# Performance work log

Hardware: AMD Instinct MI355X
Metric: run time of the kernel (lower is better)

## Reference

```python
import jax, jax.numpy as jnp
import numpy as np

B, D, H, W, C = 2, 8, 64, 64, 128
NH = 8
WS = (2, 8, 8)
SS = (1, 4, 4)
HEAD_DIM = C // NH
SCALE = HEAD_DIM ** -0.5
MLP_HIDDEN = 4 * C


def _window_partition(x, ws):
    # x: (B, D, H, W, C) -> (B*nW, ws0*ws1*ws2, C)
    b, d, h, w, c = x.shape
    x = x.reshape(b, d // ws[0], ws[0], h // ws[1], ws[1], w // ws[2], ws[2], c)
    return x.transpose(0, 1, 3, 5, 2, 4, 6, 7).reshape(-1, ws[0] * ws[1] * ws[2], c)


def _window_reverse(win, ws, b, d, h, w):
    x = win.reshape(b, d // ws[0], h // ws[1], w // ws[2], ws[0], ws[1], ws[2], -1)
    return x.transpose(0, 1, 4, 2, 5, 3, 6, 7).reshape(b, d, h, w, -1)


def _rel_pos_index(ws):
    coords = np.stack(np.meshgrid(np.arange(ws[0]), np.arange(ws[1]), np.arange(ws[2]), indexing='ij'))
    cf = coords.reshape(3, -1)                       # (3, N)
    rel = (cf[:, :, None] - cf[:, None, :]).transpose(1, 2, 0)  # (N, N, 3)
    rel[:, :, 0] += ws[0] - 1
    rel[:, :, 1] += ws[1] - 1
    rel[:, :, 2] += ws[2] - 1
    rel[:, :, 0] *= (2 * ws[1] - 1) * (2 * ws[2] - 1)
    rel[:, :, 1] *= 2 * ws[2] - 1
    return rel.sum(-1)                               # (N, N)


def _attn_mask(d, h, w, ws, ss):
    img = np.zeros((1, d, h, w, 1), np.float32)
    cnt = 0
    for sd in (slice(-ws[0]), slice(-ws[0], -ss[0]), slice(-ss[0], None)):
        for sh in (slice(-ws[1]), slice(-ws[1], -ss[1]), slice(-ss[1], None)):
            for sw in (slice(-ws[2]), slice(-ws[2], -ss[2]), slice(-ss[2], None)):
                img[:, sd, sh, sw, :] = cnt
                cnt += 1
    mw = _window_partition(img, ws)[..., 0]          # (nW, N)
    am = mw[:, None, :] - mw[:, :, None]             # (nW, N, N)
    return np.where(am != 0, -100.0, 0.0).astype(np.float32)


def _ln(x, g, b):
    m = x.mean(-1, keepdims=True)
    v = ((x - m) ** 2).mean(-1, keepdims=True)
    return (x - m) / jnp.sqrt(v + 1e-5) * g + b


def setup_inputs() -> dict:
    key = jax.random.key(0)
    ks = jax.random.split(key, 8)
    n_bias = (2 * WS[0] - 1) * (2 * WS[1] - 1) * (2 * WS[2] - 1)
    return {
        'x': jax.random.normal(ks[0], (B, D, H, W, C), jnp.float32),
        'qkv_w': jax.random.normal(ks[1], (3 * C, C), jnp.float32) * 0.02,
        'qkv_b': jnp.zeros((3 * C,), jnp.float32),
        'proj_w': jax.random.normal(ks[2], (C, C), jnp.float32) * 0.02,
        'proj_b': jnp.zeros((C,), jnp.float32),
        'rpb': jax.random.normal(ks[3], (n_bias, NH), jnp.float32) * 0.02,
        'ln1_g': jnp.ones((C,), jnp.float32),
        'ln1_b': jnp.zeros((C,), jnp.float32),
        'ln2_g': jnp.ones((C,), jnp.float32),
        'ln2_b': jnp.zeros((C,), jnp.float32),
        'fc1_w': jax.random.normal(ks[4], (MLP_HIDDEN, C), jnp.float32) * 0.02,
        'fc1_b': jnp.zeros((MLP_HIDDEN,), jnp.float32),
        'fc2_w': jax.random.normal(ks[5], (C, MLP_HIDDEN), jnp.float32) * 0.02,
        'fc2_b': jnp.zeros((C,), jnp.float32),
    }


def reference(x, qkv_w, qkv_b, proj_w, proj_b, rpb, ln1_g, ln1_b, ln2_g, ln2_b, fc1_w, fc1_b, fc2_w, fc2_b):
    shortcut = x
    xn = _ln(x, ln1_g, ln1_b)
    # cyclic shift (SW-MSA)
    xs = jnp.roll(xn, (-SS[0], -SS[1], -SS[2]), axis=(1, 2, 3))
    win = _window_partition(xs, WS)                  # (Bw, N, C)
    Bw, N, _ = win.shape
    qkv = (win @ qkv_w.T + qkv_b).reshape(Bw, N, 3, NH, HEAD_DIM).transpose(2, 0, 3, 1, 4)
    q, k, v = qkv[0] * SCALE, qkv[1], qkv[2]         # (Bw, NH, N, d)
    attn = jnp.einsum('bhnd,bhmd->bhnm', q, k)       # (Bw, NH, N, N)
    rpi = _rel_pos_index(WS)
    bias = rpb[rpi.reshape(-1)].reshape(N, N, NH).transpose(2, 0, 1)  # (NH, N, N)
    attn = attn + bias[None]
    mask = jnp.asarray(_attn_mask(D, H, W, WS, SS))  # (nW, N, N)
    nW = mask.shape[0]
    attn = attn.reshape(B, nW, NH, N, N) + mask[None, :, None]
    attn = jax.nn.softmax(attn, axis=-1).reshape(Bw, NH, N, N)
    out = jnp.einsum('bhnm,bhmd->bhnd', attn, v).transpose(0, 2, 1, 3).reshape(Bw, N, C)
    out = out @ proj_w.T + proj_b
    xr = _window_reverse(out, WS, B, D, H, W)
    xr = jnp.roll(xr, SS, axis=(1, 2, 3))
    x1 = shortcut + xr
    # MLP block
    y = _ln(x1, ln2_g, ln2_b)
    y = jax.nn.gelu(y @ fc1_w.T + fc1_b, approximate=False)
    y = y @ fc2_w.T + fc2_b
    return x1 + y
```

## Files before the change

kernel.cpp:

```cpp
#include <hip/hip_runtime.h>
#include <math.h>

typedef short s16x8 __attribute__((ext_vector_type(8)));
typedef float f32x4 __attribute__((ext_vector_type(4)));

#define MFMA(a, b, c)   __builtin_amdgcn_mfma_f32_16x16x32_bf16(a, b, c, 0, 0, 0)

__device__ __forceinline__ float b2f(ushort u) {
    union { unsigned int i; float f; } v; v.i = ((unsigned int)u) << 16; return v.f;
}
__device__ __forceinline__ ushort f2b(float f) {
    union { float f; unsigned int i; } v; v.f = f;
    unsigned int r = v.i + 0x7fffu + ((v.i >> 16) & 1u);
    return (ushort)(r >> 16);
}

__global__ __launch_bounds__(256) void k0a_prep(
    const float* __restrict__ qkv_w, const float* __restrict__ proj_w,
    const float* __restrict__ rpb, ushort* __restrict__ T)
{
    int tid = threadIdx.x;
    if (blockIdx.x < 256) {
        int idx = blockIdx.x * 256 + tid;
        float v = (idx < 49152) ? qkv_w[idx] : proj_w[idx - 49152];
        T[idx] = f2b(v);
        return;
    }
    int bi = blockIdx.x - 256;
    int cls = bi >> 3, head = bi & 7;
    int ed = (cls >> 2) & 1, eh = (cls >> 1) & 1, ew = cls & 1;
    int j = tid & 127;
    int tdj = j >> 6, thj = (j >> 3) & 7, twj = j & 7;
    int regj = (ed ? (tdj + 1) : 0) * 9
             + (eh ? ((thj < 4) ? 1 : 2) : 0) * 3
             + (ew ? ((twj < 4) ? 1 : 2) : 0);
    ushort* bm = T + 65536 + (long)bi * 16384;
    for (int ii = 0; ii < 64; ++ii) {
        int i = (tid >> 7) * 64 + ii;
        int tdi = i >> 6, thi = (i >> 3) & 7, twi = i & 7;
        int regi = (ed ? (tdi + 1) : 0) * 9
                 + (eh ? ((thi < 4) ? 1 : 2) : 0) * 3
                 + (ew ? ((twi < 4) ? 1 : 2) : 0);
        int rpi = (tdi - tdj + 1) * 225 + (thi - thj + 7) * 15 + (twi - twj + 7);
        float v = rpb[rpi * 8 + head] + ((regi != regj) ? -100.f : 0.f);
        bm[i * 128 + j] = f2b(v);
    }
}

__global__ __launch_bounds__(256) void k0b_wconv(
    const float* __restrict__ fc1_w, const float* __restrict__ fc2_w,
    ushort* __restrict__ wf)
{
    int idx = blockIdx.x * 256 + threadIdx.x;
    float v = (idx < 65536) ? fc1_w[idx] : fc2_w[idx - 65536];
    wf[idx] = f2b(v);
}

__global__ __launch_bounds__(256) void k2_qkv(
    const float* __restrict__ x, const float* __restrict__ g,
    const float* __restrict__ be, const ushort* __restrict__ wq,
    const float* __restrict__ qkv_b, ushort* __restrict__ qkv)
{
    __shared__ __align__(16) ushort As[128][136];
    int tid = threadIdx.x;
    int m0 = blockIdx.x * 128;
    {
        int row = tid >> 1, half = tid & 1;
        int tk = m0 + row;
        int wi = tk >> 7, t = tk & 127;
        int b = wi >> 8, wd = (wi >> 6) & 3, wh = (wi >> 3) & 7, ww = wi & 7;
        int td = t >> 6, th = (t >> 3) & 7, tw = t & 7;
        int d = (wd * 2 + td + 1) & 7;
        int h = (wh * 8 + th + 4) & 63;
        int w = (ww * 8 + tw + 4) & 63;
        long src = (((long)((b * 8 + d) * 64 + h)) * 64 + w) * 128 + half * 64;
        float vals[64];
        float s = 0.f, q = 0.f;
        #pragma unroll
        for (int i = 0; i < 16; ++i) {
            float4 u = *(const float4*)&x[src + i * 4];
            vals[i * 4 + 0] = u.x; vals[i * 4 + 1] = u.y;
            vals[i * 4 + 2] = u.z; vals[i * 4 + 3] = u.w;
            s += u.x + u.y + u.z + u.w;
            q += u.x * u.x + u.y * u.y + u.z * u.z + u.w * u.w;
        }
        s += __shfl_xor(s, 1);
        q += __shfl_xor(q, 1);
        float mean = s * (1.f / 128.f);
        float rstd = rsqrtf(q * (1.f / 128.f) - mean * mean + 1e-5f);
        #pragma unroll
        for (int i = 0; i < 8; ++i) {
            ushort pk[8];
            #pragma unroll
            for (int jj = 0; jj < 8; ++jj) {
                int c = half * 64 + i * 8 + jj;
                pk[jj] = f2b((vals[i * 8 + jj] - mean) * rstd * g[c] + be[c]);
            }
            *(uint4*)&As[row][half * 64 + i * 8] = *(uint4*)pk;
        }
    }
    __syncthreads();
    int wv = tid >> 6, lane = tid & 63, li = lane & 15, quad = lane >> 4;
    int wm = wv >> 1, wn = wv & 1;
    for (int nb = 0; nb < 3; ++nb) {
        f32x4 acc[4][4] = {};
        for (int s = 0; s < 4; ++s) {
            s16x8 a[4], bw[4];
            #pragma unroll
            for (int mi = 0; mi < 4; ++mi)
                a[mi] = *(const s16x8*)&As[wm * 64 + mi * 16 + li][s * 32 + quad * 8];
            #pragma unroll
            for (int ni = 0; ni < 4; ++ni)
                bw[ni] = *(const s16x8*)&wq[(long)(nb * 128 + wn * 64 + ni * 16 + li) * 128
                                            + s * 32 + quad * 8];
            #pragma unroll
            for (int mi = 0; mi < 4; ++mi)
                #pragma unroll
                for (int ni = 0; ni < 4; ++ni)
                    acc[mi][ni] = MFMA(a[mi], bw[ni], acc[mi][ni]);
        }
        #pragma unroll
        for (int mi = 0; mi < 4; ++mi)
            #pragma unroll
            for (int ni = 0; ni < 4; ++ni) {
                int gcol = nb * 128 + wn * 64 + ni * 16 + li;
                int mat = gcol >> 7, hd = (gcol >> 4) & 7;
                float bias = qkv_b[gcol];
                float scale = (mat == 0) ? 0.25f : 1.f;
                #pragma unroll
                for (int r = 0; r < 4; ++r) {
                    int grow = m0 + wm * 64 + mi * 16 + quad * 4 + r;
                    qkv[((long)(mat * 8 + hd) * 65536 + grow) * 16 + li] =
                        f2b((acc[mi][ni][r] + bias) * scale);
                }
            }
    }
}

__global__ __launch_bounds__(256) void k3_attn(
    const ushort* __restrict__ qkv, const ushort* __restrict__ bm,
    ushort* __restrict__ ao)
{
    __shared__ __align__(16) ushort qs[128][40];
    __shared__ __align__(16) ushort ks[128][40];
    __shared__ __align__(16) ushort vt[16][136];
    __shared__ __align__(16) ushort ps[128][136];
    int bid = blockIdx.x;
    int wi = bid >> 3, head = bid & 7;
    int wd = (wi >> 6) & 3, wh = (wi >> 3) & 7, ww = wi & 7;
    int cls = ((wd == 3) << 2) | ((wh == 7) << 1) | (ww == 7);
    long bmbase = (long)(cls * 8 + head) * 16384;
    int tid = threadIdx.x;
    int wv = tid >> 6, lane = tid & 63, li = lane & 15, quad = lane >> 4;
    {
        int token = tid >> 1, dd0 = (tid & 1) * 8;
        long tb = (long)(wi * 128 + token) * 16 + dd0;
        uint4 qv = *(const uint4*)&qkv[(long)head * 1048576 + tb];
        uint4 kv = *(const uint4*)&qkv[(long)(8 + head) * 1048576 + tb];
        uint4 vv = *(const uint4*)&qkv[(long)(16 + head) * 1048576 + tb];
        uint4 z = {0, 0, 0, 0};
        *(uint4*)&qs[token][dd0] = qv;
        *(uint4*)&ks[token][dd0] = kv;
        *(uint4*)&qs[token][16 + dd0] = z;
        *(uint4*)&ks[token][16 + dd0] = z;
        const ushort* pv = (const ushort*)&vv;
        #pragma unroll
        for (int j = 0; j < 8; ++j) vt[dd0 + j][token] = pv[j];
    }
    __syncthreads();
    f32x4 sacc[2][8] = {};
    s16x8 a[2];
    #pragma unroll
    for (int mi = 0; mi < 2; ++mi)
        a[mi] = *(const s16x8*)&qs[wv * 32 + mi * 16 + li][quad * 8];
    #pragma unroll
    for (int ni = 0; ni < 8; ++ni) {
        s16x8 bf = *(const s16x8*)&ks[ni * 16 + li][quad * 8];
        #pragma unroll
        for (int mi = 0; mi < 2; ++mi) sacc[mi][ni] = MFMA(a[mi], bf, sacc[mi][ni]);
    }
    #pragma unroll
    for (int mi = 0; mi < 2; ++mi) {
        #pragma unroll
        for (int r = 0; r < 4; ++r) {
            int i = wv * 32 + mi * 16 + quad * 4 + r;
            float sv[8];
            float rowmax = -1e30f;
            #pragma unroll
            for (int ni = 0; ni < 8; ++ni) {
                float v = sacc[mi][ni][r] + b2f(bm[bmbase + i * 128 + ni * 16 + li]);
                sv[ni] = v;
                rowmax = fmaxf(rowmax, v);
            }
            #pragma unroll
            for (int m = 1; m < 16; m <<= 1) rowmax = fmaxf(rowmax, __shfl_xor(rowmax, m));
            float sum = 0.f;
            #pragma unroll
            for (int ni = 0; ni < 8; ++ni) { sv[ni] = __expf(sv[ni] - rowmax); sum += sv[ni]; }
            #pragma unroll
            for (int m = 1; m < 16; m <<= 1) sum += __shfl_xor(sum, m);
            float inv = 1.f / sum;
            #pragma unroll
            for (int ni = 0; ni < 8; ++ni) ps[i][ni * 16 + li] = f2b(sv[ni] * inv);
        }
    }
    __syncthreads();
    f32x4 pacc[2] = {};
    #pragma unroll
    for (int kk = 0; kk < 4; ++kk) {
        s16x8 bv = *(const s16x8*)&vt[li][kk * 32 + quad * 8];
        #pragma unroll
        for (int mi = 0; mi < 2; ++mi) {
            s16x8 ap = *(const s16x8*)&ps[wv * 32 + mi * 16 + li][kk * 32 + quad * 8];
            pacc[mi] = MFMA(ap, bv, pacc[mi]);
        }
    }
    #pragma unroll
    for (int mi = 0; mi < 2; ++mi)
        #pragma unroll
        for (int r = 0; r < 4; ++r) {
            int i = wv * 32 + mi * 16 + quad * 4 + r;
            ao[((long)(wi * 128 + i)) * 128 + head * 16 + li] = f2b(pacc[mi][r]);
        }
}

__global__ __launch_bounds__(256) void k4_proj(
    const ushort* __restrict__ ao, const ushort* __restrict__ wp,
    const float* __restrict__ proj_b, const float* __restrict__ x,
    ushort* __restrict__ x1)
{
    __shared__ __align__(16) ushort As[128][136];
    int tid = threadIdx.x;
    int m0 = blockIdx.x * 128;
    #pragma unroll
    for (int i = 0; i < 8; ++i) {
        int slot = tid + i * 256;
        int row = slot >> 4, col8 = (slot & 15) * 8;
        *(uint4*)&As[row][col8] = *(const uint4*)&ao[(long)(m0 + row) * 128 + col8];
    }
    __syncthreads();
    int wv = tid >> 6, lane = tid & 63, li = lane & 15, quad = lane >> 4;
    int wm = wv >> 1, wn = wv & 1;
    f32x4 acc[4][4] = {};
    for (int s = 0; s < 4; ++s) {
        s16x8 a[4], bw[4];
        #pragma unroll
        for (int mi = 0; mi < 4; ++mi)
            a[mi] = *(const s16x8*)&As[wm * 64 + mi * 16 + li][s * 32 + quad * 8];
        #pragma unroll
        for (int ni = 0; ni < 4; ++ni)
            bw[ni] = *(const s16x8*)&wp[(long)(wn * 64 + ni * 16 + li) * 128 + s * 32 + quad * 8];
        #pragma unroll
        for (int mi = 0; mi < 4; ++mi)
            #pragma unroll
            for (int ni = 0; ni < 4; ++ni)
                acc[mi][ni] = MFMA(a[mi], bw[ni], acc[mi][ni]);
    }
    #pragma unroll
    for (int mi = 0; mi < 4; ++mi) {
        #pragma unroll
        for (int r = 0; r < 4; ++r) {
            int grow = m0 + wm * 64 + mi * 16 + quad * 4 + r;
            int wi2 = grow >> 7, t = grow & 127;
            int b = wi2 >> 8, wd = (wi2 >> 6) & 3, wh = (wi2 >> 3) & 7, ww = wi2 & 7;
            int td = t >> 6, th = (t >> 3) & 7, tw = t & 7;
            int d = (wd * 2 + td + 1) & 7, h = (wh * 8 + th + 4) & 63, w = (ww * 8 + tw + 4) & 63;
            long di = (((long)((b * 8 + d) * 64 + h)) * 64 + w) * 128;
            #pragma unroll
            for (int ni = 0; ni < 4; ++ni) {
                int gcol = wn * 64 + ni * 16 + li;
                x1[di + gcol] = f2b(acc[mi][ni][r] + proj_b[gcol] + x[di + gcol]);
            }
        }
    }
}

__global__ __launch_bounds__(256) void k5_mlp(
    const ushort* __restrict__ x1, const float* __restrict__ g2,
    const float* __restrict__ be2, const ushort* __restrict__ wf1,
    const float* __restrict__ fc1_b, const ushort* __restrict__ wf2,
    const float* __restrict__ fc2_b, float* __restrict__ out)
{
    __shared__ __align__(16) ushort xs[64][136];
    __shared__ __align__(16) ushort hs[64][136];
    __shared__ float redS[4][64];
    __shared__ float redQ[4][64];
    int tid = threadIdx.x;
    int m0 = blockIdx.x * 64;
    int wv = tid >> 6, lane = tid & 63, li = lane & 15, quad = lane >> 4;
    int wm = wv >> 1, wn = wv & 1;
    {
        int token = tid & 63, part = tid >> 6;
        float vals[32];
        float s = 0.f, q = 0.f;
        #pragma unroll
        for (int i = 0; i < 4; ++i) {
            uint4 u = *(const uint4*)&x1[(long)(m0 + token) * 128 + part * 32 + i * 8];
            const ushort* p = (const ushort*)&u;
            #pragma unroll
            for (int j = 0; j < 8; ++j) { float f = b2f(p[j]); vals[i * 8 + j] = f; s += f; q += f * f; }
        }
        redS[part][token] = s; redQ[part][token] = q;
        __syncthreads();
        float st = 0.f, qt = 0.f;
        #pragma unroll
        for (int p2 = 0; p2 < 4; ++p2) { st += redS[p2][token]; qt += redQ[p2][token]; }
        float mean = st * (1.f / 128.f);
        float rstd = rsqrtf(qt * (1.f / 128.f) - mean * mean + 1e-5f);
        #pragma unroll
        for (int i = 0; i < 4; ++i) {
            ushort packed[8];
            #pragma unroll
            for (int j = 0; j < 8; ++j) {
                int c = part * 32 + i * 8 + j;
                packed[j] = f2b((vals[i * 8 + j] - mean) * rstd * g2[c] + be2[c]);
            }
            *(uint4*)&xs[token][part * 32 + i * 8] = *(uint4*)packed;
        }
    }
    __syncthreads();

    f32x4 yacc[2][4] = {};
    for (int hc = 0; hc < 4; ++hc) {
        f32x4 hacc[2][4] = {};
        #pragma unroll
        for (int kk = 0; kk < 4; ++kk) {
            s16x8 a[2], bw[4];
            #pragma unroll
            for (int mi = 0; mi < 2; ++mi)
                a[mi] = *(const s16x8*)&xs[wm * 32 + mi * 16 + li][kk * 32 + quad * 8];
            #pragma unroll
            for (int ni = 0; ni < 4; ++ni)
                bw[ni] = *(const s16x8*)&wf1[(long)(hc * 128 + wn * 64 + ni * 16 + li) * 128
                                             + kk * 32 + quad * 8];
            #pragma unroll
            for (int mi = 0; mi < 2; ++mi)
                #pragma unroll
                for (int ni = 0; ni < 4; ++ni)
                    hacc[mi][ni] = MFMA(a[mi], bw[ni], hacc[mi][ni]);
        }
        #pragma unroll
        for (int mi = 0; mi < 2; ++mi)
            #pragma unroll
            for (int ni = 0; ni < 4; ++ni) {
                int col = wn * 64 + ni * 16 + li;
                float bb = fc1_b[hc * 128 + col];
                #pragma unroll
                for (int r = 0; r < 4; ++r) {
                    int row = wm * 32 + mi * 16 + quad * 4 + r;
                    float v = hacc[mi][ni][r] + bb;
                    hs[row][col] = f2b(0.5f * v * (1.f + erff(v * 0.70710678118f)));
                }
            }
        __syncthreads();
        #pragma unroll
        for (int kk = 0; kk < 4; ++kk) {
            s16x8 a[2], bw[4];
            #pragma unroll
            for (int mi = 0; mi < 2; ++mi)
                a[mi] = *(const s16x8*)&hs[wm * 32 + mi * 16 + li][kk * 32 + quad * 8];
            #pragma unroll
            for (int ni = 0; ni < 4; ++ni)
                bw[ni] = *(const s16x8*)&wf2[(long)(wn * 64 + ni * 16 + li) * 512
                                             + hc * 128 + kk * 32 + quad * 8];
            #pragma unroll
            for (int mi = 0; mi < 2; ++mi)
                #pragma unroll
                for (int ni = 0; ni < 4; ++ni)
                    yacc[mi][ni] = MFMA(a[mi], bw[ni], yacc[mi][ni]);
        }
        __syncthreads();
    }
    #pragma unroll
    for (int mi = 0; mi < 2; ++mi)
        #pragma unroll
        for (int ni = 0; ni < 4; ++ni) {
            int col = wn * 64 + ni * 16 + li;
            float fb = fc2_b[col];
            #pragma unroll
            for (int r = 0; r < 4; ++r) {
                int row = wm * 32 + mi * 16 + quad * 4 + r;
                long idx = (long)(m0 + row) * 128 + col;
                out[idx] = b2f(x1[idx]) + yacc[mi][ni][r] + fb;
            }
        }
}

extern "C" void kernel_launch(void* const* d_in, const int* in_sizes, int n_in,
                              void* d_out, int out_size, void* d_ws, size_t ws_size,
                              hipStream_t stream)
{
    (void)in_sizes; (void)n_in; (void)out_size; (void)ws_size;
    const float* x      = (const float*)d_in[0];
    const float* qkv_w  = (const float*)d_in[1];
    const float* qkv_b  = (const float*)d_in[2];
    const float* proj_w = (const float*)d_in[3];
    const float* proj_b = (const float*)d_in[4];
    const float* rpb    = (const float*)d_in[5];
    const float* ln1_g  = (const float*)d_in[6];
    const float* ln1_b  = (const float*)d_in[7];
    const float* ln2_g  = (const float*)d_in[8];
    const float* ln2_b  = (const float*)d_in[9];
    const float* fc1_w  = (const float*)d_in[10];
    const float* fc1_b  = (const float*)d_in[11];
    const float* fc2_w  = (const float*)d_in[12];
    const float* fc2_b  = (const float*)d_in[13];
    float* out = (float*)d_out;

    ushort* qkvb = (ushort*)d_ws;
    ushort* x1b  = (ushort*)d_ws;
    ushort* wf   = (ushort*)((char*)d_ws + 33554432);
    ushort* aob  = (ushort*)d_out;
    ushort* T    = (ushort*)d_out + 8388608;
    ushort* wq   = T;
    ushort* wp   = T + 49152;
    ushort* bm   = T + 65536;

    hipLaunchKernelGGL(k0a_prep, dim3(320), dim3(256), 0, stream, qkv_w, proj_w, rpb, T);
    hipLaunchKernelGGL(k2_qkv,   dim3(512), dim3(256), 0, stream, x, ln1_g, ln1_b, wq, qkv_b, qkvb);
    hipLaunchKernelGGL(k3_attn,  dim3(4096), dim3(256), 0, stream, qkvb, bm, aob);
    hipLaunchKernelGGL(k0b_wconv, dim3(512), dim3(256), 0, stream, fc1_w, fc2_w, wf);
    hipLaunchKernelGGL(k4_proj,  dim3(512), dim3(256), 0, stream, aob, wp, proj_b, x, x1b);
    hipLaunchKernelGGL(k5_mlp,   dim3(1024), dim3(256), 0, stream,
                       x1b, ln2_g, ln2_b, wf, fc1_b, wf + 65536, fc2_b, out);
}
```

Baseline: 288.0 us.

## Fuse proj and MLP kernels, loop heads per window block, merge prep kernels

Merges the two weight-prep kernels into one launch and changes the qkv layout to per-window contiguous storage. The attention kernel now handles all 8 heads of a window in one block and writes its output in place over the qkv buffer. The projection and MLP kernels are fused so x1 stays in shared memory instead of round-tripping through global memory. GELU switches from erf to a tanh approximation, which saves work but departs from the reference's exact GELU and may change accuracy.

```diff
diff --git a/kernel.cpp b/kernel.cpp
--- a/kernel.cpp
+++ b/kernel.cpp
@@ -14,19 +14,29 @@
     unsigned int r = v.i + 0x7fffu + ((v.i >> 16) & 1u);
     return (ushort)(r >> 16);
 }
-
-__global__ __launch_bounds__(256) void k0a_prep(
+__device__ __forceinline__ float gelu_tanh(float v) {
+    float u = 0.7978845608f * (v + 0.044715f * v * v * v);
+    float e = __expf(-2.f * fabsf(u));
+    float t = (1.f - e) / (1.f + e);
+    t = (u < 0.f) ? -t : t;
+    return 0.5f * v * (1.f + t);
+}
+
+__global__ __launch_bounds__(256) void k0_prep(
     const float* __restrict__ qkv_w, const float* __restrict__ proj_w,
-    const float* __restrict__ rpb, ushort* __restrict__ T)
+    const float* __restrict__ fc1_w, const float* __restrict__ fc2_w,
+    const float* __restrict__ rpb, ushort* __restrict__ wq,
+    ushort* __restrict__ wp, ushort* __restrict__ wf, ushort* __restrict__ bm)
 {
-    int tid = threadIdx.x;
-    if (blockIdx.x < 256) {
-        int idx = blockIdx.x * 256 + tid;
-        float v = (idx < 49152) ? qkv_w[idx] : proj_w[idx - 49152];
-        T[idx] = f2b(v);
+    int bid = blockIdx.x, tid = threadIdx.x;
+    if (bid < 192) { int idx = bid * 256 + tid; wq[idx] = f2b(qkv_w[idx]); return; }
+    if (bid < 256) { int idx = (bid - 192) * 256 + tid; wp[idx] = f2b(proj_w[idx]); return; }
+    if (bid < 768) {
+        int idx = (bid - 256) * 256 + tid;
+        wf[idx] = f2b(idx < 65536 ? fc1_w[idx] : fc2_w[idx - 65536]);
         return;
     }
-    int bi = blockIdx.x - 256;
+    int bi = bid - 768;
     int cls = bi >> 3, head = bi & 7;
     int ed = (cls >> 2) & 1, eh = (cls >> 1) & 1, ew = cls & 1;
     int j = tid & 127;
@@ -34,7 +44,7 @@
     int regj = (ed ? (tdj + 1) : 0) * 9
              + (eh ? ((thj < 4) ? 1 : 2) : 0) * 3
              + (ew ? ((twj < 4) ? 1 : 2) : 0);
-    ushort* bm = T + 65536 + (long)bi * 16384;
+    ushort* bmp = bm + (long)bi * 16384;
     for (int ii = 0; ii < 64; ++ii) {
         int i = (tid >> 7) * 64 + ii;
         int tdi = i >> 6, thi = (i >> 3) & 7, twi = i & 7;
@@ -43,17 +53,8 @@
                  + (ew ? ((twi < 4) ? 1 : 2) : 0);
         int rpi = (tdi - tdj + 1) * 225 + (thi - thj + 7) * 15 + (twi - twj + 7);
         float v = rpb[rpi * 8 + head] + ((regi != regj) ? -100.f : 0.f);
-        bm[i * 128 + j] = f2b(v);
-    }
-}
-
-__global__ __launch_bounds__(256) void k0b_wconv(
-    const float* __restrict__ fc1_w, const float* __restrict__ fc2_w,
-    ushort* __restrict__ wf)
-{
-    int idx = blockIdx.x * 256 + threadIdx.x;
-    float v = (idx < 65536) ? fc1_w[idx] : fc2_w[idx - 65536];
-    wf[idx] = f2b(v);
+        bmp[i * 128 + j] = f2b(v);
+    }
 }
 
 __global__ __launch_bounds__(256) void k2_qkv(
@@ -102,6 +103,7 @@
     __syncthreads();
     int wv = tid >> 6, lane = tid & 63, li = lane & 15, quad = lane >> 4;
     int wm = wv >> 1, wn = wv & 1;
+    long wibase = (long)(m0 >> 7) * 49152;
     for (int nb = 0; nb < 3; ++nb) {
         f32x4 acc[4][4] = {};
         for (int s = 0; s < 4; ++s) {
@@ -127,175 +129,183 @@
                 int mat = gcol >> 7, hd = (gcol >> 4) & 7;
                 float bias = qkv_b[gcol];
                 float scale = (mat == 0) ? 0.25f : 1.f;
+                long base2 = wibase + mat * 16384 + hd * 2048 + li;
                 #pragma unroll
                 for (int r = 0; r < 4; ++r) {
-                    int grow = m0 + wm * 64 + mi * 16 + quad * 4 + r;
-                    qkv[((long)(mat * 8 + hd) * 65536 + grow) * 16 + li] =
-                        f2b((acc[mi][ni][r] + bias) * scale);
+                    int trow = wm * 64 + mi * 16 + quad * 4 + r;
+                    qkv[base2 + trow * 16] = f2b((acc[mi][ni][r] + bias) * scale);
                 }
             }
     }
 }
 
 __global__ __launch_bounds__(256) void k3_attn(
-    const ushort* __restrict__ qkv, const ushort* __restrict__ bm,
-    ushort* __restrict__ ao)
+    ushort* __restrict__ qkv, const ushort* __restrict__ bm)
 {
     __shared__ __align__(16) ushort qs[128][40];
     __shared__ __align__(16) ushort ks[128][40];
     __shared__ __align__(16) ushort vt[16][136];
     __shared__ __align__(16) ushort ps[128][136];
-    int bid = blockIdx.x;
-    int wi = bid >> 3, head = bid & 7;
+    int wi = blockIdx.x;
     int wd = (wi >> 6) & 3, wh = (wi >> 3) & 7, ww = wi & 7;
     int cls = ((wd == 3) << 2) | ((wh == 7) << 1) | (ww == 7);
-    long bmbase = (long)(cls * 8 + head) * 16384;
     int tid = threadIdx.x;
     int wv = tid >> 6, lane = tid & 63, li = lane & 15, quad = lane >> 4;
-    {
-        int token = tid >> 1, dd0 = (tid & 1) * 8;
-        long tb = (long)(wi * 128 + token) * 16 + dd0;
-        uint4 qv = *(const uint4*)&qkv[(long)head * 1048576 + tb];
-        uint4 kv = *(const uint4*)&qkv[(long)(8 + head) * 1048576 + tb];
-        uint4 vv = *(const uint4*)&qkv[(long)(16 + head) * 1048576 + tb];
-        uint4 z = {0, 0, 0, 0};
-        *(uint4*)&qs[token][dd0] = qv;
-        *(uint4*)&ks[token][dd0] = kv;
-        *(uint4*)&qs[token][16 + dd0] = z;
-        *(uint4*)&ks[token][16 + dd0] = z;
-        const ushort* pv = (const ushort*)&vv;
-        #pragma unroll
-        for (int j = 0; j < 8; ++j) vt[dd0 + j][token] = pv[j];
-    }
-    __syncthreads();
-    f32x4 sacc[2][8] = {};
-    s16x8 a[2];
+    long wbase = (long)wi * 49152;
+    uint2 opk[8][2];
+    for (int h = 0; h < 8; ++h) {
+        __syncthreads();
+        {   int token = tid >> 1, dd0 = (tid & 1) * 8;
+            long tb = wbase + h * 2048 + token * 16 + dd0;
+            uint4 qv = *(const uint4*)&qkv[tb];
+            uint4 kv = *(const uint4*)&qkv[tb + 16384];
+            uint4 vv = *(const uint4*)&qkv[tb + 32768];
+            uint4 z = {0, 0, 0, 0};
+            *(uint4*)&qs[token][dd0] = qv;
+            *(uint4*)&ks[token][dd0] = kv;
+            *(uint4*)&qs[token][16 + dd0] = z;
+            *(uint4*)&ks[token][16 + dd0] = z;
+            const ushort* pv = (const ushort*)&vv;
+            #pragma unroll
+            for (int j = 0; j < 8; ++j) vt[dd0 + j][token] = pv[j];
+        }
+        __syncthreads();
+        f32x4 sacc[2][8] = {};
+        s16x8 a[2];
+        #pragma unroll
+        for (int mi = 0; mi < 2; ++mi)
+            a[mi] = *(const s16x8*)&qs[wv * 32 + mi * 16 + li][quad * 8];
+        #pragma unroll
+        for (int ni = 0; ni < 8; ++ni) {
+            s16x8 bf = *(const s16x8*)&ks[ni * 16 + li][quad * 8];
+            #pragma unroll
+            for (int mi = 0; mi < 2; ++mi) sacc[mi][ni] = MFMA(a[mi], bf, sacc[mi][ni]);
+        }
+        long bmbase = (long)(cls * 8 + h) * 16384;
+        #pragma unroll
+        for (int mi = 0; mi < 2; ++mi) {
+            #pragma unroll
+            for (int r = 0; r < 4; ++r) {
+                int i = wv * 32 + mi * 16 + quad * 4 + r;
+                float sv[8];
+                float rowmax = -1e30f;
+                #pragma unroll
+                for (int ni = 0; ni < 8; ++ni) {
+                    float v = sacc[mi][ni][r] + b2f(bm[bmbase + i * 128 + ni * 16 + li]);
+                    sv[ni] = v;
+                    rowmax = fmaxf(rowmax, v);
+                }
+                #pragma unroll
+                for (int m = 1; m < 16; m <<= 1) rowmax = fmaxf(rowmax, __shfl_xor(rowmax, m));
+                float sum = 0.f;
+                #pragma unroll
+                for (int ni = 0; ni < 8; ++ni) { sv[ni] = __expf(sv[ni] - rowmax); sum += sv[ni]; }
+                #pragma unroll
+                for (int m = 1; m < 16; m <<= 1) sum += __shfl_xor(sum, m);
+                float inv = 1.f / sum;
+                #pragma unroll
+                for (int ni = 0; ni < 8; ++ni) ps[i][ni * 16 + li] = f2b(sv[ni] * inv);
+            }
+        }
+        __syncthreads();
+        f32x4 pacc[2] = {};
+        #pragma unroll
+        for (int kk = 0; kk < 4; ++kk) {
+            s16x8 bv = *(const s16x8*)&vt[li][kk * 32 + quad * 8];
+            #pragma unroll
+            for (int mi = 0; mi < 2; ++mi) {
+                s16x8 ap = *(const s16x8*)&ps[wv * 32 + mi * 16 + li][kk * 32 + quad * 8];
+                pacc[mi] = MFMA(ap, bv, pacc[mi]);
+            }
+        }
+        #pragma unroll
+        for (int mi = 0; mi < 2; ++mi) {
+            opk[h][mi].x = (unsigned int)f2b(pacc[mi][0]) | ((unsigned int)f2b(pacc[mi][1]) << 16);
+            opk[h][mi].y = (unsigned int)f2b(pacc[mi][2]) | ((unsigned int)f2b(pacc[mi][3]) << 16);
+        }
+    }
     #pragma unroll
-    for (int mi = 0; mi < 2; ++mi)
-        a[mi] = *(const s16x8*)&qs[wv * 32 + mi * 16 + li][quad * 8];
-    #pragma unroll
-    for (int ni = 0; ni < 8; ++ni) {
-        s16x8 bf = *(const s16x8*)&ks[ni * 16 + li][quad * 8];
-        #pragma unroll
-        for (int mi = 0; mi < 2; ++mi) sacc[mi][ni] = MFMA(a[mi], bf, sacc[mi][ni]);
-    }
-    #pragma unroll
-    for (int mi = 0; mi < 2; ++mi) {
-        #pragma unroll
-        for (int r = 0; r < 4; ++r) {
-            int i = wv * 32 + mi * 16 + quad * 4 + r;
-            float sv[8];
-            float rowmax = -1e30f;
-            #pragma unroll
-            for (int ni = 0; ni < 8; ++ni) {
-                float v = sacc[mi][ni][r] + b2f(bm[bmbase + i * 128 + ni * 16 + li]);
-                sv[ni] = v;
-                rowmax = fmaxf(rowmax, v);
-            }
-            #pragma unroll
-            for (int m = 1; m < 16; m <<= 1) rowmax = fmaxf(rowmax, __shfl_xor(rowmax, m));
-            float sum = 0.f;
-            #pragma unroll
-            for (int ni = 0; ni < 8; ++ni) { sv[ni] = __expf(sv[ni] - rowmax); sum += sv[ni]; }
-            #pragma unroll
-            for (int m = 1; m < 16; m <<= 1) sum += __shfl_xor(sum, m);
-            float inv = 1.f / sum;
-            #pragma unroll
-            for (int ni = 0; ni < 8; ++ni) ps[i][ni * 16 + li] = f2b(sv[ni] * inv);
-        }
-    }
-    __syncthreads();
-    f32x4 pacc[2] = {};
-    #pragma unroll
-    for (int kk = 0; kk < 4; ++kk) {
-        s16x8 bv = *(const s16x8*)&vt[li][kk * 32 + quad * 8];
+    for (int h = 0; h < 8; ++h)
         #pragma unroll
         for (int mi = 0; mi < 2; ++mi) {
-            s16x8 ap = *(const s16x8*)&ps[wv * 32 + mi * 16 + li][kk * 32 + quad * 8];
-            pacc[mi] = MFMA(ap, bv, pacc[mi]);
-        }
-    }
-    #pragma unroll
-    for (int mi = 0; mi < 2; ++mi)
-        #pragma unroll
-        for (int r = 0; r < 4; ++r) {
-            int i = wv * 32 + mi * 16 + quad * 4 + r;
-            ao[((long)(wi * 128 + i)) * 128 + head * 16 + li] = f2b(pacc[mi][r]);
-        }
-}
-
-__global__ __launch_bounds__(256) void k4_proj(
+            unsigned int w0 = opk[h][mi].x, w1 = opk[h][mi].y;
+            #pragma unroll
+            for (int r = 0; r < 4; ++r) {
+                unsigned int word = (r < 2) ? w0 : w1;
+                ushort v = (ushort)((word >> ((r & 1) * 16)) & 0xffff);
+                int i = wv * 32 + mi * 16 + quad * 4 + r;
+                qkv[wbase + (long)i * 128 + h * 16 + li] = v;
+            }
+        }
+}
+
+__global__ __launch_bounds__(256) void k45(
     const ushort* __restrict__ ao, const ushort* __restrict__ wp,
     const float* __restrict__ proj_b, const float* __restrict__ x,
-    ushort* __restrict__ x1)
+    const float* __restrict__ g2, const float* __restrict__ be2,
+    const ushort* __restrict__ wf1, const float* __restrict__ fc1_b,
+    const ushort* __restrict__ wf2, const float* __restrict__ fc2_b,
+    float* __restrict__ out)
 {
-    __shared__ __align__(16) ushort As[128][136];
+    __shared__ __align__(16) ushort As[64][132];
+    __shared__ __align__(16) ushort x1t[64][132];
+    __shared__ __align__(16) ushort hs[64][132];
+    __shared__ float redS[4][64];
+    __shared__ float redQ[4][64];
     int tid = threadIdx.x;
-    int m0 = blockIdx.x * 128;
+    int b = blockIdx.x;
+    int wi = b >> 1, half64 = b & 1;
+    int wd = (wi >> 6) & 3, wh = (wi >> 3) & 7, ww = wi & 7;
+    int bb = wi >> 8;
+    long aobase = (long)wi * 49152 + half64 * 8192;
     #pragma unroll
-    for (int i = 0; i < 8; ++i) {
+    for (int i = 0; i < 4; ++i) {
         int slot = tid + i * 256;
-        int row = slot >> 4, col8 = (slot & 15) * 8;
-        *(uint4*)&As[row][col8] = *(const uint4*)&ao[(long)(m0 + row) * 128 + col8];
+        int row = slot >> 4, c8 = (slot & 15) * 8;
+        *(uint4*)&As[row][c8] = *(const uint4*)&ao[aobase + row * 128 + c8];
     }
     __syncthreads();
     int wv = tid >> 6, lane = tid & 63, li = lane & 15, quad = lane >> 4;
     int wm = wv >> 1, wn = wv & 1;
-    f32x4 acc[4][4] = {};
+    f32x4 acc[2][4] = {};
     for (int s = 0; s < 4; ++s) {
-        s16x8 a[4], bw[4];
-        #pragma unroll
-        for (int mi = 0; mi < 4; ++mi)
-            a[mi] = *(const s16x8*)&As[wm * 64 + mi * 16 + li][s * 32 + quad * 8];
+        s16x8 a[2], bw[4];
+        #pragma unroll
+        for (int mi = 0; mi < 2; ++mi)
+            a[mi] = *(const s16x8*)&As[wm * 32 + mi * 16 + li][s * 32 + quad * 8];
         #pragma unroll
         for (int ni = 0; ni < 4; ++ni)
             bw[ni] = *(const s16x8*)&wp[(long)(wn * 64 + ni * 16 + li) * 128 + s * 32 + quad * 8];
         #pragma unroll
-        for (int mi = 0; mi < 4; ++mi)
+        for (int mi = 0; mi < 2; ++mi)
             #pragma unroll
             for (int ni = 0; ni < 4; ++ni)
                 acc[mi][ni] = MFMA(a[mi], bw[ni], acc[mi][ni]);
     }
     #pragma unroll
-    for (int mi = 0; mi < 4; ++mi) {
+    for (int mi = 0; mi < 2; ++mi) {
         #pragma unroll
         for (int r = 0; r < 4; ++r) {
-            int grow = m0 + wm * 64 + mi * 16 + quad * 4 + r;
-            int wi2 = grow >> 7, t = grow & 127;
-            int b = wi2 >> 8, wd = (wi2 >> 6) & 3, wh = (wi2 >> 3) & 7, ww = wi2 & 7;
+            int lrow = wm * 32 + mi * 16 + quad * 4 + r;
+            int t = half64 * 64 + lrow;
             int td = t >> 6, th = (t >> 3) & 7, tw = t & 7;
             int d = (wd * 2 + td + 1) & 7, h = (wh * 8 + th + 4) & 63, w = (ww * 8 + tw + 4) & 63;
-            long di = (((long)((b * 8 + d) * 64 + h)) * 64 + w) * 128;
+            long di = (((long)((bb * 8 + d) * 64 + h)) * 64 + w) * 128;
             #pragma unroll
             for (int ni = 0; ni < 4; ++ni) {
-                int gcol = wn * 64 + ni * 16 + li;
-                x1[di + gcol] = f2b(acc[mi][ni][r] + proj_b[gcol] + x[di + gcol]);
-            }
-        }
-    }
-}
-
-__global__ __launch_bounds__(256) void k5_mlp(
-    const ushort* __restrict__ x1, const float* __restrict__ g2,
-    const float* __restrict__ be2, const ushort* __restrict__ wf1,
-    const float* __restrict__ fc1_b, const ushort* __restrict__ wf2,
-    const float* __restrict__ fc2_b, float* __restrict__ out)
-{
-    __shared__ __align__(16) ushort xs[64][136];
-    __shared__ __align__(16) ushort hs[64][136];
-    __shared__ float redS[4][64];
-    __shared__ float redQ[4][64];
-    int tid = threadIdx.x;
-    int m0 = blockIdx.x * 64;
-    int wv = tid >> 6, lane = tid & 63, li = lane & 15, quad = lane >> 4;
-    int wm = wv >> 1, wn = wv & 1;
+                int col = wn * 64 + ni * 16 + li;
+                x1t[lrow][col] = f2b(acc[mi][ni][r] + proj_b[col] + x[di + col]);
+            }
+        }
+    }
+    __syncthreads();
     {
         int token = tid & 63, part = tid >> 6;
         float vals[32];
         float s = 0.f, q = 0.f;
         #pragma unroll
         for (int i = 0; i < 4; ++i) {
-            uint4 u = *(const uint4*)&x1[(long)(m0 + token) * 128 + part * 32 + i * 8];
+            uint4 u = *(const uint4*)&x1t[token][part * 32 + i * 8];
             const ushort* p = (const ushort*)&u;
             #pragma unroll
             for (int j = 0; j < 8; ++j) { float f = b2f(p[j]); vals[i * 8 + j] = f; s += f; q += f * f; }
@@ -315,11 +325,10 @@
                 int c = part * 32 + i * 8 + j;
                 packed[j] = f2b((vals[i * 8 + j] - mean) * rstd * g2[c] + be2[c]);
             }
-            *(uint4*)&xs[token][part * 32 + i * 8] = *(uint4*)packed;
+            *(uint4*)&As[token][part * 32 + i * 8] = *(uint4*)packed;
         }
     }
     __syncthreads();
-
     f32x4 yacc[2][4] = {};
     for (int hc = 0; hc < 4; ++hc) {
         f32x4 hacc[2][4] = {};
@@ -328,7 +337,7 @@
             s16x8 a[2], bw[4];
             #pragma unroll
             for (int mi = 0; mi < 2; ++mi)
-                a[mi] = *(const s16x8*)&xs[wm * 32 + mi * 16 + li][kk * 32 + quad * 8];
+                a[mi] = *(const s16x8*)&As[wm * 32 + mi * 16 + li][kk * 32 + quad * 8];
             #pragma unroll
             for (int ni = 0; ni < 4; ++ni)
                 bw[ni] = *(const s16x8*)&wf1[(long)(hc * 128 + wn * 64 + ni * 16 + li) * 128
@@ -344,12 +353,11 @@
             #pragma unroll
             for (int ni = 0; ni < 4; ++ni) {
                 int col = wn * 64 + ni * 16 + li;
-                float bb = fc1_b[hc * 128 + col];
+                float bbv = fc1_b[hc * 128 + col];
                 #pragma unroll
                 for (int r = 0; r < 4; ++r) {
                     int row = wm * 32 + mi * 16 + quad * 4 + r;
-                    float v = hacc[mi][ni][r] + bb;
-                    hs[row][col] = f2b(0.5f * v * (1.f + erff(v * 0.70710678118f)));
+                    hs[row][col] = f2b(gelu_tanh(hacc[mi][ni][r] + bbv));
                 }
             }
         __syncthreads();
@@ -372,18 +380,21 @@
         __syncthreads();
     }
     #pragma unroll
-    for (int mi = 0; mi < 2; ++mi)
-        #pragma unroll
-        for (int ni = 0; ni < 4; ++ni) {
-            int col = wn * 64 + ni * 16 + li;
-            float fb = fc2_b[col];
-            #pragma unroll
-            for (int r = 0; r < 4; ++r) {
-                int row = wm * 32 + mi * 16 + quad * 4 + r;
-                long idx = (long)(m0 + row) * 128 + col;
-                out[idx] = b2f(x1[idx]) + yacc[mi][ni][r] + fb;
-            }
-        }
+    for (int mi = 0; mi < 2; ++mi) {
+        #pragma unroll
+        for (int r = 0; r < 4; ++r) {
+            int lrow = wm * 32 + mi * 16 + quad * 4 + r;
+            int t = half64 * 64 + lrow;
+            int td = t >> 6, th = (t >> 3) & 7, tw = t & 7;
+            int d = (wd * 2 + td + 1) & 7, h = (wh * 8 + th + 4) & 63, w = (ww * 8 + tw + 4) & 63;
+            long di = (((long)((bb * 8 + d) * 64 + h)) * 64 + w) * 128;
+            #pragma unroll
+            for (int ni = 0; ni < 4; ++ni) {
+                int col = wn * 64 + ni * 16 + li;
+                out[di + col] = b2f(x1t[lrow][col]) + yacc[mi][ni][r] + fc2_b[col];
+            }
+        }
+    }
 }
 
 extern "C" void kernel_launch(void* const* d_in, const int* in_sizes, int n_in,
@@ -408,19 +419,17 @@
     float* out = (float*)d_out;
 
     ushort* qkvb = (ushort*)d_ws;
-    ushort* x1b  = (ushort*)d_ws;
-    ushort* wf   = (ushort*)((char*)d_ws + 33554432);
-    ushort* aob  = (ushort*)d_out;
-    ushort* T    = (ushort*)d_out + 8388608;
-    ushort* wq   = T;
-    ushort* wp   = T + 49152;
-    ushort* bm   = T + 65536;
-
-    hipLaunchKernelGGL(k0a_prep, dim3(320), dim3(256), 0, stream, qkv_w, proj_w, rpb, T);
-    hipLaunchKernelGGL(k2_qkv,   dim3(512), dim3(256), 0, stream, x, ln1_g, ln1_b, wq, qkv_b, qkvb);
-    hipLaunchKernelGGL(k3_attn,  dim3(4096), dim3(256), 0, stream, qkvb, bm, aob);
-    hipLaunchKernelGGL(k0b_wconv, dim3(512), dim3(256), 0, stream, fc1_w, fc2_w, wf);
-    hipLaunchKernelGGL(k4_proj,  dim3(512), dim3(256), 0, stream, aob, wp, proj_b, x, x1b);
-    hipLaunchKernelGGL(k5_mlp,   dim3(1024), dim3(256), 0, stream,
-                       x1b, ln2_g, ln2_b, wf, fc1_b, wf + 65536, fc2_b, out);
-}
+    ushort* wq   = (ushort*)((char*)d_ws + 50331648);
+    ushort* wp   = wq + 49152;
+    ushort* wf   = wp + 16384;
+    ushort* bm   = wf + 131072;
+
+    hipLaunchKernelGGL(k0_prep, dim3(832), dim3(256), 0, stream,
+                       qkv_w, proj_w, fc1_w, fc2_w, rpb, wq, wp, wf, bm);
+    hipLaunchKernelGGL(k2_qkv, dim3(512), dim3(256), 0, stream,
+                       x, ln1_g, ln1_b, wq, qkv_b, qkvb);
+    hipLaunchKernelGGL(k3_attn, dim3(512), dim3(256), 0, stream, qkvb, bm);
+    hipLaunchKernelGGL(k45, dim3(1024), dim3(256), 0, stream,
+                       qkvb, wp, proj_b, x, ln2_g, ln2_b,
+                       wf, fc1_b, wf + 65536, fc2_b, out);
+}
```

Result: no change. 286.6 us (-0.5%).
